# Optimization experiments

Hardware: AMD Instinct MI355X
Metric: run time of the kernel (lower is better)

## Reference

```python
import jax, jax.numpy as jnp
import numpy as np

EMBED_DIM = 512
NUM_HEADS = 8
B, L_Q, L_K = 2, 2048, 2048


def setup_inputs() -> dict:
    key = jax.random.key(0)
    ks = jax.random.split(key, 8)
    s = 0.02  # weight init scale
    return {
        "query": jax.random.normal(ks[0], (B, L_Q, EMBED_DIM), jnp.float32),
        "key":   jax.random.normal(ks[1], (B, L_K, EMBED_DIM), jnp.float32),
        "value": jax.random.normal(ks[2], (B, L_K, EMBED_DIM), jnp.float32),
        "wq": jax.random.normal(ks[3], (EMBED_DIM, EMBED_DIM), jnp.float32) * s,
        "wk": jax.random.normal(ks[4], (EMBED_DIM, EMBED_DIM), jnp.float32) * s,
        "wv": jax.random.normal(ks[5], (EMBED_DIM, EMBED_DIM), jnp.float32) * s,
        "bq": jnp.zeros((EMBED_DIM,), jnp.float32),
        "bk": jnp.zeros((EMBED_DIM,), jnp.float32),
        "bv": jnp.zeros((EMBED_DIM,), jnp.float32),
        "wo": jax.random.normal(ks[6], (EMBED_DIM, EMBED_DIM), jnp.float32) * s,
        "bo": jnp.zeros((EMBED_DIM,), jnp.float32),
    }


def _prob_sparse_mask(query, key, num_heads):
    # Faithful to _prob_QK: max-mean sparsity score, top-k query selection,
    # gather of reduced queries, reduced QK matmul (vectorized, no python loops).
    Bq, Lq, D = query.shape
    Lk = key.shape[1]
    dh = D // num_heads
    n_top = int(np.log(Lk))  # int(np.ceil/np.log) as in source forward: int(np.log(L_K))
    Q = query.reshape(Bq, Lq, num_heads, dh)
    K = key.reshape(Bq, Lk, num_heads, dh)
    Qh = jnp.transpose(Q, (0, 2, 1, 3))                      # [B,H,Lq,dh]
    # NOTE: source does K.transpose(1,2).reshape(B,H,D,L_K) -- a reshape, not a
    # transpose of the last two dims. We replicate that exactly.
    Kr = jnp.transpose(K, (0, 2, 1, 3)).reshape(Bq, num_heads, dh, Lk)  # [B,H,dh,Lk]
    QK = jnp.einsum('bhqd,bhdk->bhqk', Qh, Kr)               # [B,H,Lq,Lk]
    M = QK.max(-1) - QK.sum(-1) / Lk                         # max-mean score [B,H,Lq]
    _, M_top = jax.lax.top_k(M, n_top)                       # [B,H,n_top]
    Q_red = jnp.take_along_axis(Qh, M_top[..., None], axis=2)  # [B,H,n_top,dh]
    QK_red = jnp.einsum('bhtd,bhdk->bhtk', Q_red, Kr)        # [B,H,n_top,Lk]
    # Scatter reduced rows back into a full additive attn mask (zeros elsewhere).
    mask = jnp.zeros((Bq, num_heads, Lq, Lk), QK.dtype)
    bi = jnp.arange(Bq)[:, None, None]
    hi = jnp.arange(num_heads)[None, :, None]
    return mask.at[bi, hi, M_top].set(QK_red)


def reference(query, key, value, wq, wk, wv, bq, bk, bv, wo, bo):
    Bq, Lq, D = query.shape
    Lk = key.shape[1]
    H = NUM_HEADS
    dh = D // H
    mask = _prob_sparse_mask(query, key, H)                  # [B,H,Lq,Lk]
    q = (query @ wq.T + bq).reshape(Bq, Lq, H, dh).transpose(0, 2, 1, 3)
    k = (key @ wk.T + bk).reshape(Bq, Lk, H, dh).transpose(0, 2, 1, 3)
    v = (value @ wv.T + bv).reshape(Bq, Lk, H, dh).transpose(0, 2, 1, 3)
    scores = jnp.einsum('bhqd,bhkd->bhqk', q, k) * (dh ** -0.5) + mask
    attn = jax.nn.softmax(scores, axis=-1)                   # dropout inactive (eval)
    out = jnp.einsum('bhqk,bhkd->bhqd', attn, v)
    out = out.transpose(0, 2, 1, 3).reshape(Bq, Lq, D)
    return out @ wo.T + bo
```

## Files before the change

kernel.cpp:

```cpp
#include <hip/hip_runtime.h>
#include <type_traits>

#define DEV static __device__ __forceinline__

typedef short s16;
typedef __attribute__((ext_vector_type(8))) short short8;
typedef __attribute__((ext_vector_type(4))) float f32x4;
typedef __attribute__((ext_vector_type(16))) float f32x16;

#define NB 2
#define NH 8
#define SL 2048
#define DM 512
#define DH 64
#define NTOP 7
#define NCAND 16
#define LOG2E 1.4426950408889634f
#define NROWS (NB*NH*SL)
#define FSPLIT 4
#define SSPLIT 4

DEV short f2bf(float x){
  union { float f; unsigned u; } v; v.f = x;
  unsigned r = v.u + 0x7fffu + ((v.u >> 16) & 1u);
  return (short)(r >> 16);
}
DEV f32x4 mfma16(short8 a, short8 b, f32x4 c){
  return __builtin_amdgcn_mfma_f32_16x16x32_bf16(a, b, c, 0, 0, 0);
}
DEV f32x16 mfma32(short8 a, short8 b, f32x16 c){
  return __builtin_amdgcn_mfma_f32_32x32x16_bf16(a, b, c, 0, 0, 0);
}
DEV unsigned cvtpk(float lo, float hi){
  unsigned r;
  asm("v_cvt_pk_bf16_f32 %0, %1, %2" : "=v"(r) : "v"(lo), "v"(hi));
  return r;
}
DEV void gl2lds16(const s16* g, s16* l){
  __builtin_amdgcn_global_load_lds(
      (const __attribute__((address_space(1))) unsigned*)g,
      (__attribute__((address_space(3))) unsigned*)l, 16, 0, 0);
}

__global__ void prep_kernel(const float* __restrict__ query, const float* __restrict__ key,
    const float* __restrict__ value,
    const float* __restrict__ wq, const float* __restrict__ wk,
    const float* __restrict__ wv, const float* __restrict__ wo,
    s16* __restrict__ xq, s16* __restrict__ xk, s16* __restrict__ xv,
    s16* __restrict__ khat,
    s16* __restrict__ wqb, s16* __restrict__ wkb, s16* __restrict__ wvb, s16* __restrict__ wob){
  const int nbb = (NB*SL*DM)/256;
  const int wbb = (DM*DM)/256;
  __shared__ s16 thi[64][66];
  int bid = blockIdx.x;
  int t = threadIdx.x;
  if (bid < nbb){ int i = bid*256 + t; xq[i] = f2bf(query[i]); return; }
  bid -= nbb;
  if (bid < nbb){ int i = bid*256 + t; xk[i] = f2bf(key[i]); return; }
  bid -= nbb;
  if (bid < nbb){ int i = bid*256 + t; xv[i] = f2bf(value[i]); return; }
  bid -= nbb;
  if (bid < 512){
    int k6 = bid & 31, h = (bid >> 5) & 7, b = bid >> 8;
    int kl = t & 63, dq = t >> 6;
    #pragma unroll
    for (int dd = 0; dd < 16; ++dd){
      int d = dd*4 + dq;
      thi[d][kl] = f2bf(key[((size_t)b*SL + d*32 + k6)*DM + h*DH + kl]);
    }
    __syncthreads();
    int d2 = t & 63, kq = t >> 6;
    size_t obase = (((size_t)(b*NH + h))*SL + (size_t)k6*64)*DH;
    #pragma unroll
    for (int kk = 0; kk < 16; ++kk){
      int kl2 = kk*4 + kq;
      khat[obase + (size_t)kl2*DH + d2] = thi[d2][kl2];
    }
    return;
  }
  bid -= 512;
  if (bid < wbb){ int i = bid*256 + t; wqb[i] = f2bf(wq[i]); return; }
  bid -= wbb;
  if (bid < wbb){ int i = bid*256 + t; wkb[i] = f2bf(wk[i]); return; }
  bid -= wbb;
  if (bid < wbb){ int i = bid*256 + t; wvb[i] = f2bf(wv[i]); return; }
  bid -= wbb;
  if (bid < wbb){ int i = bid*256 + t; wob[i] = f2bf(wo[i]); return; }
}

__global__ __launch_bounds__(256) void vpt_kernel(const s16* __restrict__ Vp, s16* __restrict__ VpT){
  __shared__ s16 tl[64][66];
  int bid = blockIdx.x;
  int k6 = bid & 31, h = (bid >> 5) & 7, b = bid >> 8;
  int t = threadIdx.x;
  int d = t & 63, kq = t >> 6;
  #pragma unroll
  for (int kk = 0; kk < 16; ++kk){
    int kl = kk*4 + kq;
    tl[kl][d] = Vp[((size_t)b*SL + k6*64 + kl)*DM + h*DH + d];
  }
  __syncthreads();
  int kl2 = t & 63, dq = t >> 6;
  size_t obase = ((size_t)(b*NH + h))*DH*SL + (size_t)k6*64;
  #pragma unroll
  for (int dd = 0; dd < 16; ++dd){
    int d2 = dd*4 + dq;
    VpT[obase + (size_t)d2*SL + kl2] = tl[kl2][d2];
  }
}

template<int OUTF32>
DEV void gemm_body(const s16* __restrict__ A, const s16* __restrict__ Bw,
        const float* __restrict__ bias, void* __restrict__ Cout, int bid, int tid, float scale){
  __shared__ __align__(16) s16 Abuf[2][128*64];
  __shared__ __align__(16) s16 Bbuf[2][64*64];
  int nt = bid >> 3, ot = bid & 7;
  int w = tid >> 6, l = tid & 63;
  int lr = l & 15, lg = l >> 4;
  int n0 = nt*128, o0 = ot*64;
  auto stage = [&](int cur, int kg){
    #pragma unroll
    for (int i = 0; i < 4; ++i){
      int r = w*32 + i*8 + (l>>3);
      int cs = (l&7) ^ (r&7);
      gl2lds16(A + (size_t)(n0 + r)*DM + kg + cs*8, &Abuf[cur][(w*32 + i*8)*64]);
    }
    #pragma unroll
    for (int i = 0; i < 2; ++i){
      int r = w*16 + i*8 + (l>>3);
      int cs = (l&7) ^ (r&7);
      gl2lds16(Bw + (size_t)(o0 + r)*DM + kg + cs*8, &Bbuf[cur][(w*16 + i*8)*64]);
    }
  };
  f32x4 acc[2][4] = {};
  stage(0, 0);
  __syncthreads();
  const int NIT = DM/64;
  for (int it = 0; it < NIT; ++it){
    int cur = it & 1;
    if (it + 1 < NIT) stage(cur^1, (it+1)*64);
    #pragma unroll
    for (int kc = 0; kc < 2; ++kc){
      short8 a0 = *(const short8*)&Abuf[cur][(w*32 +      lr)*64 + ((kc*4+lg) ^ (lr&7))*8];
      short8 a1 = *(const short8*)&Abuf[cur][(w*32 + 16 + lr)*64 + ((kc*4+lg) ^ (lr&7))*8];
      #pragma unroll
      for (int c = 0; c < 4; ++c){
        short8 bf = *(const short8*)&Bbuf[cur][(c*16 + lr)*64 + ((kc*4+lg) ^ (lr&7))*8];
        acc[0][c] = mfma16(a0, bf, acc[0][c]);
        acc[1][c] = mfma16(a1, bf, acc[1][c]);
      }
    }
    __syncthreads();
  }
  #pragma unroll
  for (int sub = 0; sub < 2; ++sub)
    #pragma unroll
    for (int c = 0; c < 4; ++c){
      int col = o0 + c*16 + lr;
      float bb = bias[col];
      #pragma unroll
      for (int j = 0; j < 4; ++j){
        int row = n0 + w*32 + sub*16 + lg*4 + j;
        float v = (acc[sub][c][j] + bb)*scale;
        if (OUTF32) ((float*)Cout)[(size_t)row*DM + col] = v;
        else        ((s16*) Cout)[(size_t)row*DM + col] = f2bf(v);
      }
    }
}

__global__ __launch_bounds__(256) void gemm_proj(const s16* __restrict__ Aq, const s16* __restrict__ Ak,
        const s16* __restrict__ Av, const s16* __restrict__ Wq, const s16* __restrict__ Wk,
        const s16* __restrict__ Wv, const float* __restrict__ bq, const float* __restrict__ bk,
        const float* __restrict__ bv, s16* __restrict__ Oq, s16* __restrict__ Ok, s16* __restrict__ Ov){
  int which = blockIdx.x >> 8;
  const s16* A  = which == 0 ? Aq : which == 1 ? Ak : Av;
  const s16* Bw = which == 0 ? Wq : which == 1 ? Wk : Wv;
  const float* bias = which == 0 ? bq : which == 1 ? bk : bv;
  s16* C = which == 0 ? Oq : which == 1 ? Ok : Ov;
  float scale = which == 0 ? 0.125f*LOG2E : 1.0f;
  gemm_body<0>(A, Bw, bias, C, blockIdx.x & 255, threadIdx.x, scale);
}

__global__ __launch_bounds__(256) void gemm_out(const s16* __restrict__ A, const s16* __restrict__ Bw,
        const float* __restrict__ bias, float* __restrict__ Cout){
  gemm_body<1>(A, Bw, bias, Cout, blockIdx.x, threadIdx.x, 1.0f);
}

__global__ __launch_bounds__(512) void stats_kernel(const s16* __restrict__ xq,
        const s16* __restrict__ khat, float* __restrict__ Mmx, float* __restrict__ Msm){
  __shared__ __align__(16) s16 Hbuf[2][64*64];
  int bid = blockIdx.x;
  int s = bid & 3, qt = (bid >> 2) & 15, h = (bid >> 6) & 7, b = bid >> 9;
  int tid = threadIdx.x;
  int w = tid >> 6, l = tid & 63;
  int lr = l & 15, lg = l >> 4;
  int dx = lr & 7;
  int q0 = qt*128 + w*16;
  const s16* qp = xq + ((size_t)b*SL + q0 + lr)*DM + h*DH + lg*8;
  short8 qh0 = *(const short8*)qp;
  short8 qh1 = *(const short8*)(qp + 32);
  const s16* kb = khat + ((size_t)b*NH + h)*SL*DH;
  const s16* hR0 = &Hbuf[0][lr*64 + ((lg      ^ dx)*8)];
  const s16* hR1 = &Hbuf[0][lr*64 + (((4+lg) ^ dx)*8)];
  int rS = tid >> 3;
  int slot = tid & 7;
  int cs = slot ^ (rS & 7);
  int kbeg = s*(SL/SSPLIT);
  const int NT = (SL/SSPLIT)/64;
  f32x4 hreg;
  auto loadr = [&](int t){
    hreg = *(const f32x4*)(kb + (size_t)(kbeg + t*64 + rS)*DH + cs*8);
  };
  auto writer = [&](int buf){
    *(f32x4*)&Hbuf[buf][rS*64 + slot*8] = hreg;
  };
  float mx = -1e30f, sm = 0.f;
  auto body = [&](auto CURC){
    constexpr int CUR = decltype(CURC)::value;
    #pragma unroll
    for (int t = 0; t < 4; ++t){
      short8 kh0 = *(const short8*)(hR0 + CUR*4096 + t*1024);
      short8 kh1 = *(const short8*)(hR1 + CUR*4096 + t*1024);
      f32x4 sacc = {};
      sacc = mfma16(kh0, qh0, sacc);
      sacc = mfma16(kh1, qh1, sacc);
      #pragma unroll
      for (int j = 0; j < 4; ++j){ mx = fmaxf(mx, sacc[j]); sm += sacc[j]; }
    }
  };
  loadr(0);
  writer(0);
  loadr(1);
  __syncthreads();
  auto step = [&](auto TC){
    constexpr int T = decltype(TC)::value;
    if constexpr (T + 1 < NT) writer((T+1)&1);
    if constexpr (T + 2 < NT) loadr(T+2);
    body(std::integral_constant<int, T&1>{});
    __syncthreads();
  };
  step(std::integral_constant<int,0>{}); step(std::integral_constant<int,1>{});
  step(std::integral_constant<int,2>{}); step(std::integral_constant<int,3>{});
  step(std::integral_constant<int,4>{}); step(std::integral_constant<int,5>{});
  step(std::integral_constant<int,6>{}); step(std::integral_constant<int,7>{});
  mx = fmaxf(mx, __shfl_xor(mx, 16));
  mx = fmaxf(mx, __shfl_xor(mx, 32));
  sm += __shfl_xor(sm, 16);
  sm += __shfl_xor(sm, 32);
  if (lg == 0){
    size_t row = ((size_t)b*NH + h)*SL + q0 + lr;
    Mmx[(size_t)s*NROWS + row] = mx;
    Msm[(size_t)s*NROWS + row] = sm;
  }
}

__global__ __launch_bounds__(256) void topk_kernel(const float* __restrict__ Mmx,
        const float* __restrict__ Msm, int* __restrict__ candidx, int* __restrict__ rowsel){
  int bh = blockIdx.x;
  int t = threadIdx.x;
  int w = t >> 6, l = t & 63;
  __shared__ float smv[SL];
  __shared__ float rv[4];
  __shared__ int   ri[4];
  size_t base = (size_t)bh*SL;
  for (int i = t; i < SL; i += 256){
    float mx = Mmx[base + i];
    float sm = Msm[base + i];
    #pragma unroll
    for (int s = 1; s < SSPLIT; ++s){
      mx = fmaxf(mx, Mmx[(size_t)s*NROWS + base + i]);
      sm += Msm[(size_t)s*NROWS + base + i];
    }
    smv[i] = mx - sm*(1.0f/SL);
    rowsel[base + i] = -1;
  }
  __syncthreads();
  for (int tt = 0; tt < NCAND; ++tt){
    float bvv = -1e38f; int bi = SL;
    for (int i = t; i < SL; i += 256){
      float v = smv[i];
      if (v > bvv){ bvv = v; bi = i; }
    }
    #pragma unroll
    for (int off = 32; off >= 1; off >>= 1){
      float ov = __shfl_xor(bvv, off);
      int oi = __shfl_xor(bi, off);
      if (ov > bvv || (ov == bvv && oi < bi)){ bvv = ov; bi = oi; }
    }
    if (l == 0){ rv[w] = bvv; ri[w] = bi; }
    __syncthreads();
    if (t == 0){
      float bv2 = rv[0]; int bi2 = ri[0];
      #pragma unroll
      for (int ww = 1; ww < 4; ++ww)
        if (rv[ww] > bv2 || (rv[ww] == bv2 && ri[ww] < bi2)){ bv2 = rv[ww]; bi2 = ri[ww]; }
      candidx[bh*NCAND + tt] = bi2;
      smv[bi2] = -1e38f;
    }
    __syncthreads();
  }
}

__global__ __launch_bounds__(256) void cand_kernel(const float* __restrict__ query,
        const float* __restrict__ key, const int* __restrict__ candidx,
        float* __restrict__ candrows, float* __restrict__ cmx, float* __restrict__ csm){
  __shared__ float tile[64][65];
  __shared__ float qs[NCAND][64];
  int bid = blockIdx.x;
  int k6 = bid & 31, h = (bid >> 5) & 7, b = bid >> 8;
  int bh = b*NH + h;
  int t = threadIdx.x;
  int kl = t & 63, w = t >> 6;
  for (int i = t; i < NCAND*64; i += 256){
    int tt = i >> 6, d = i & 63;
    qs[tt][d] = query[((size_t)b*SL + candidx[bh*NCAND + tt])*DM + h*DH + d];
  }
  #pragma unroll
  for (int dd = 0; dd < 16; ++dd){
    int d = dd*4 + w;
    tile[d][kl] = key[((size_t)b*SL + d*32 + k6)*DM + h*DH + kl];
  }
  __syncthreads();
  for (int tt = w; tt < NCAND; tt += 4){
    float acc = 0.f;
    #pragma unroll
    for (int d = 0; d < 64; ++d)
      acc = fmaf(qs[tt][d], tile[d][kl], acc);
    candrows[((size_t)bh*NCAND + tt)*SL + k6*64 + kl] = acc*LOG2E;
    float mx = acc, sm = acc;
    #pragma unroll
    for (int off = 1; off < 64; off <<= 1){
      mx = fmaxf(mx, __shfl_xor(mx, off));
      sm += __shfl_xor(sm, off);
    }
    if (kl == 0){
      cmx[((size_t)bh*NCAND + tt)*32 + k6] = mx;
      csm[((size_t)bh*NCAND + tt)*32 + k6] = sm;
    }
  }
}

__global__ __launch_bounds__(64) void topsel_kernel(const float* __restrict__ cmx,
        const float* __restrict__ csm, const int* __restrict__ candidx, int* __restrict__ rowsel){
  int bh = blockIdx.x;
  int l = threadIdx.x;
  __shared__ float Mex[NCAND];
  if (l < NCAND){
    float mx = -1e38f, sm = 0.f;
    #pragma unroll 4
    for (int p = 0; p < 32; ++p){
      mx = fmaxf(mx, cmx[((size_t)bh*NCAND + l)*32 + p]);
      sm += csm[((size_t)bh*NCAND + l)*32 + p];
    }
    Mex[l] = mx - sm*(1.0f/SL);
  }
  __syncthreads();
  if (l == 0){
    unsigned used = 0;
    for (int tt = 0; tt < NTOP; ++tt){
      float bv = -1e38f; int bslot = 0; int brow = 1 << 30;
      for (int c = 0; c < NCAND; ++c){
        if (used & (1u << c)) continue;
        int row = candidx[bh*NCAND + c];
        float v = Mex[c];
        if (v > bv || (v == bv && row < brow)){ bv = v; bslot = c; brow = row; }
      }
      used |= 1u << bslot;
      rowsel[(size_t)bh*SL + brow] = bslot;
    }
  }
}

__global__ __launch_bounds__(256, 3) void flash_kernel(const s16* __restrict__ Qp,
        const s16* __restrict__ Kp, const s16* __restrict__ VpT,
        const float* __restrict__ candrows, const int* __restrict__ rowsel,
        float* __restrict__ Opart, float* __restrict__ lpart){
  __shared__ __align__(16) s16 SB[4*64*64];
  int bid = blockIdx.x;
  int s = bid & 3, qt = (bid >> 2) & 15, h = (bid >> 6) & 7, b = bid >> 9;
  int tid = threadIdx.x;
  int w = tid >> 6, l = tid & 63;
  int ln = l & 31, lh = l >> 5;
  int q0 = qt*128 + w*32;
  int bh = b*NH + h;
  const s16* qp = Qp + ((size_t)b*SL + q0 + ln)*DM + h*DH + lh*8;
  short8 bq[4];
  #pragma unroll
  for (int kc = 0; kc < 4; ++kc) bq[kc] = *(const short8*)(qp + kc*16);
  int sel = rowsel[(size_t)bh*SL + q0 + ln];
  const float* mrow = candrows + ((size_t)bh*NCAND + (sel >= 0 ? sel : 0))*SL;
  const s16* kpb = Kp + (size_t)b*SL*DM + h*DH;
  const s16* vtb = VpT + (size_t)bh*DH*SL;
  const s16* kR[2][4];
  #pragma unroll
  for (int g = 0; g < 2; ++g)
    #pragma unroll
    for (int kc = 0; kc < 4; ++kc)
      kR[g][kc] = &SB[(g*32 + ln)*64 + ((((kc*2 + lh) ^ (ln & 7) ^ ((ln >> 3) & 3))*8))];
  int r8 = l >> 3;
  int slot = l & 7;
  int cs = slot ^ r8 ^ w;
  int kbeg = s*(SL/FSPLIT);
  const int NT = (SL/FSPLIT)/64;
  f32x4 kreg[2], vreg[2];
  auto loadr = [&](int t){
    int kg = kbeg + t*64;
    #pragma unroll
    for (int c = 0; c < 2; ++c){
      int r = c*32 + w*8 + r8;
      kreg[c] = *(const f32x4*)(kpb + (size_t)(kg + r)*DM + cs*8);
      vreg[c] = *(const f32x4*)(vtb + (size_t)r*SL + kg + cs*8);
    }
  };
  auto writer = [&](int buf){
    #pragma unroll
    for (int c = 0; c < 2; ++c){
      int r = c*32 + w*8 + r8;
      *(f32x4*)&SB[(size_t)buf*4096 + r*64 + slot*8] = kreg[c];
      *(f32x4*)&SB[8192 + (size_t)buf*4096 + r*64 + slot*8] = vreg[c];
    }
  };
  short8 ones;
  #pragma unroll
  for (int i = 0; i < 8; ++i) ones[i] = (short)0x3F80;
  f32x16 accO[2] = {};
  f32x16 accL = {};
  auto body = [&](auto CURC, int k0){
    constexpr int CB = decltype(CURC)::value * 8192;
    f32x16 S[2] = {};
    __builtin_amdgcn_s_setprio(1);
    #pragma unroll
    for (int g = 0; g < 2; ++g)
      #pragma unroll
      for (int kc = 0; kc < 4; ++kc){
        short8 kf = *(const short8*)((const char*)kR[g][kc] + CB);
        S[g] = mfma32(kf, bq[kc], S[g]);
      }
    __builtin_amdgcn_s_setprio(0);
    if (sel >= 0){
      #pragma unroll
      for (int g = 0; g < 2; ++g)
        #pragma unroll
        for (int rq = 0; rq < 4; ++rq)
          #pragma unroll
          for (int j = 0; j < 4; ++j)
            S[g][rq*4 + j] += mrow[k0 + g*32 + rq*8 + lh*4 + j];
    }
    #pragma unroll
    for (int g = 0; g < 2; ++g)
      #pragma unroll
      for (int e = 0; e < 16; ++e)
        S[g][e] = exp2f(S[g][e]);
    unsigned W[2][8];
    #pragma unroll
    for (int g = 0; g < 2; ++g)
      #pragma unroll
      for (int t = 0; t < 8; ++t)
        W[g][t] = cvtpk(S[g][2*t], S[g][2*t+1]);
    short8 pf[4];
    #pragma unroll
    for (int kc = 0; kc < 4; ++kc){
      int g = kc >> 1, j = kc & 1;
      unsigned a0 = W[g][4*j + 0], a1 = W[g][4*j + 2];
      asm("v_permlane32_swap_b32 %0, %1" : "+v"(a0), "+v"(a1));
      unsigned b0 = W[g][4*j + 1], b1 = W[g][4*j + 3];
      asm("v_permlane32_swap_b32 %0, %1" : "+v"(b0), "+v"(b1));
      union { unsigned u[4]; short8 s8; } uu;
      uu.u[0] = a0; uu.u[1] = b0; uu.u[2] = a1; uu.u[3] = b1;
      pf[kc] = uu.s8;
    }
    __builtin_amdgcn_s_setprio(1);
    #pragma unroll
    for (int kc = 0; kc < 4; ++kc)
      accL = mfma32(ones, pf[kc], accL);
    #pragma unroll
    for (int dg = 0; dg < 2; ++dg)
      #pragma unroll
      for (int kc = 0; kc < 4; ++kc){
        short8 vf = *(const short8*)((const char*)kR[dg][kc] + CB + 16384);
        accO[dg] = mfma32(vf, pf[kc], accO[dg]);
      }
    __builtin_amdgcn_s_setprio(0);
  };
  loadr(0);
  writer(0);
  loadr(1);
  __syncthreads();
  auto step = [&](auto TC){
    constexpr int T = decltype(TC)::value;
    if constexpr (T + 1 < NT) writer((T+1)&1);
    if constexpr (T + 2 < NT) loadr(T+2);
    body(std::integral_constant<int, T&1>{}, kbeg + T*64);
    __syncthreads();
  };
  step(std::integral_constant<int,0>{}); step(std::integral_constant<int,1>{});
  step(std::integral_constant<int,2>{}); step(std::integral_constant<int,3>{});
  step(std::integral_constant<int,4>{}); step(std::integral_constant<int,5>{});
  step(std::integral_constant<int,6>{}); step(std::integral_constant<int,7>{});
  size_t row = (size_t)bh*SL + q0 + ln;
  float* Op = Opart + ((size_t)s*NROWS + row)*DH;
  #pragma unroll
  for (int dg = 0; dg < 2; ++dg)
    #pragma unroll
    for (int rq = 0; rq < 4; ++rq){
      f32x4 v = { accO[dg][rq*4+0], accO[dg][rq*4+1], accO[dg][rq*4+2], accO[dg][rq*4+3] };
      *(f32x4*)(Op + dg*32 + rq*8 + lh*4) = v;
    }
  if (lh == 0)
    lpart[(size_t)s*NROWS + row] = accL[0];
}

__global__ __launch_bounds__(256) void flash_combine(const float* __restrict__ Opart,
        const float* __restrict__ lpart, s16* __restrict__ outh){
  int row = blockIdx.x*4 + (threadIdx.x >> 6);
  int d = threadIdx.x & 63;
  float L = 0.f, o = 0.f;
  #pragma unroll
  for (int s = 0; s < FSPLIT; ++s){
    L += lpart[(size_t)s*NROWS + row];
    o += Opart[((size_t)s*NROWS + row)*DH + d];
  }
  o /= L;
  int b = row >> 14, h = (row >> 11) & 7, q = row & (SL - 1);
  outh[((size_t)b*SL + q)*DM + h*DH + d] = f2bf(o);
}

extern "C" void kernel_launch(void* const* d_in, const int* in_sizes, int n_in,
                              void* d_out, int out_size, void* d_ws, size_t ws_size,
                              hipStream_t stream){
  (void)in_sizes; (void)n_in; (void)out_size;
  const float* query = (const float*)d_in[0];
  const float* key   = (const float*)d_in[1];
  const float* value = (const float*)d_in[2];
  const float* wq    = (const float*)d_in[3];
  const float* wk    = (const float*)d_in[4];
  const float* wv    = (const float*)d_in[5];
  const float* bq    = (const float*)d_in[6];
  const float* bk    = (const float*)d_in[7];
  const float* bv    = (const float*)d_in[8];
  const float* wo    = (const float*)d_in[9];
  const float* bo    = (const float*)d_in[10];

  const size_t NE = (size_t)NB*SL*DM;
  const size_t WE = (size_t)DM*DM;

  char* p = (char*)d_ws;
  size_t off = 0;
  auto alloc = [&](size_t n)->char*{ char* r = p + off; off += (n + 255) & ~(size_t)255; return r; };
  s16* wob = (s16*)alloc(WE*2);
  s16* Qp  = (s16*)alloc(NE*2);
  s16* Kp  = (s16*)alloc(NE*2);
  s16* VpT = (s16*)alloc(NE*2);
  float* candrows = (float*)alloc((size_t)NB*NH*NCAND*SL*4);
  int* candidx  = (int*)alloc((size_t)NB*NH*NCAND*4);
  float* cmx    = (float*)alloc((size_t)NB*NH*NCAND*32*4);
  float* csm    = (float*)alloc((size_t)NB*NH*NCAND*32*4);
  int* rowsel   = (int*)alloc((size_t)NROWS*4);
  float* Mmx    = (float*)alloc((size_t)SSPLIT*NROWS*4);
  float* Msm    = (float*)alloc((size_t)SSPLIT*NROWS*4);
  float* lpart  = (float*)alloc((size_t)FSPLIT*NROWS*4);
  float* Opart  = (float*)alloc((size_t)FSPLIT*NROWS*DH*4);
  s16* outh = (s16*)alloc(NE*2);
  s16* xq   = (s16*)alloc(NE*2);
  s16* xk   = (s16*)alloc(NE*2);
  s16* xv   = (s16*)alloc(NE*2);
  s16* khat = (s16*)alloc(NE*2);
  s16* wqb = (s16*)alloc(WE*2);
  s16* wkb = (s16*)alloc(WE*2);
  s16* wvb = (s16*)alloc(WE*2);
  s16* Vp  = (s16*)alloc(NE*2);
  if (off > ws_size) return;

  const int nbb = (int)(NE/256);
  const int wbb = (int)(WE/256);
  prep_kernel<<<3*nbb + 512 + 4*wbb, 256, 0, stream>>>(query, key, value, wq, wk, wv, wo,
      xq, xk, xv, khat, wqb, wkb, wvb, wob);

  gemm_proj<<<3*256, 256, 0, stream>>>(xq, xk, xv, wqb, wkb, wvb, bq, bk, bv, Qp, Kp, Vp);
  vpt_kernel<<<512, 256, 0, stream>>>(Vp, VpT);

  stats_kernel<<<NB*NH*(SL/128)*SSPLIT, 512, 0, stream>>>(xq, khat, Mmx, Msm);
  topk_kernel<<<NB*NH, 256, 0, stream>>>(Mmx, Msm, candidx, rowsel);
  cand_kernel<<<512, 256, 0, stream>>>(query, key, candidx, candrows, cmx, csm);
  topsel_kernel<<<NB*NH, 64, 0, stream>>>(cmx, csm, candidx, rowsel);

  flash_kernel<<<NB*NH*(SL/128)*FSPLIT, 256, 0, stream>>>(Qp, Kp, VpT, candrows, rowsel,
      Opart, lpart);
  flash_combine<<<NROWS/4, 256, 0, stream>>>(Opart, lpart, outh);
  gemm_out<<<256, 256, 0, stream>>>(outh, wob, bo, (float*)d_out);
}
```

Baseline: 149.2 us.

## Halve flash key split, register-resident top-k, rolled pipeline loop

Reduces the flash attention key split from 4 to 2 partitions, so there are half as many blocks, each processing twice as many key tiles. This halves the Opart/lpart traffic the combine kernel must read, at the cost of fewer blocks to fill the GPU. The main loop becomes a rolled two-stage double-buffered loop instead of a fully unrolled sequence. The top-k kernel keeps scores in registers and rescans only the winning thread's values each round instead of rescanning shared memory, and workspace buffers are reordered.

```diff
diff --git a/kernel.cpp b/kernel.cpp
--- a/kernel.cpp
+++ b/kernel.cpp
@@ -17,7 +17,7 @@
 #define NCAND 16
 #define LOG2E 1.4426950408889634f
 #define NROWS (NB*NH*SL)
-#define FSPLIT 4
+#define FSPLIT 2
 #define SSPLIT 4
 
 DEV short f2bf(float x){
@@ -259,11 +259,14 @@
   int bh = blockIdx.x;
   int t = threadIdx.x;
   int w = t >> 6, l = t & 63;
-  __shared__ float smv[SL];
-  __shared__ float rv[4];
-  __shared__ int   ri[4];
+  __shared__ float bval[4];
+  __shared__ int   bidx[4];
+  __shared__ int   gsel;
   size_t base = (size_t)bh*SL;
-  for (int i = t; i < SL; i += 256){
+  float v[8];
+  #pragma unroll
+  for (int j = 0; j < 8; ++j){
+    int i = j*256 + t;
     float mx = Mmx[base + i];
     float sm = Msm[base + i];
     #pragma unroll
@@ -271,33 +274,40 @@
       mx = fmaxf(mx, Mmx[(size_t)s*NROWS + base + i]);
       sm += Msm[(size_t)s*NROWS + base + i];
     }
-    smv[i] = mx - sm*(1.0f/SL);
+    v[j] = mx - sm*(1.0f/SL);
     rowsel[base + i] = -1;
   }
-  __syncthreads();
+  float lv = -1e38f; int li = SL;
+  #pragma unroll
+  for (int j = 0; j < 8; ++j)
+    if (v[j] > lv){ lv = v[j]; li = j*256 + t; }
   for (int tt = 0; tt < NCAND; ++tt){
-    float bvv = -1e38f; int bi = SL;
-    for (int i = t; i < SL; i += 256){
-      float v = smv[i];
-      if (v > bvv){ bvv = v; bi = i; }
-    }
+    float cv = lv; int ci = li;
     #pragma unroll
     for (int off = 32; off >= 1; off >>= 1){
-      float ov = __shfl_xor(bvv, off);
-      int oi = __shfl_xor(bi, off);
-      if (ov > bvv || (ov == bvv && oi < bi)){ bvv = ov; bi = oi; }
-    }
-    if (l == 0){ rv[w] = bvv; ri[w] = bi; }
+      float ov = __shfl_xor(cv, off);
+      int oi = __shfl_xor(ci, off);
+      if (ov > cv || (ov == cv && oi < ci)){ cv = ov; ci = oi; }
+    }
+    if (l == 0){ bval[w] = cv; bidx[w] = ci; }
     __syncthreads();
     if (t == 0){
-      float bv2 = rv[0]; int bi2 = ri[0];
+      float bv2 = bval[0]; int bi2 = bidx[0];
       #pragma unroll
       for (int ww = 1; ww < 4; ++ww)
-        if (rv[ww] > bv2 || (rv[ww] == bv2 && ri[ww] < bi2)){ bv2 = rv[ww]; bi2 = ri[ww]; }
+        if (bval[ww] > bv2 || (bval[ww] == bv2 && bidx[ww] < bi2)){ bv2 = bval[ww]; bi2 = bidx[ww]; }
       candidx[bh*NCAND + tt] = bi2;
-      smv[bi2] = -1e38f;
+      gsel = bi2;
     }
     __syncthreads();
+    int win = gsel;
+    if ((win & 255) == t){
+      v[win >> 8] = -1e38f;
+      lv = -1e38f; li = SL;
+      #pragma unroll
+      for (int j = 0; j < 8; ++j)
+        if (v[j] > lv){ lv = v[j]; li = j*256 + t; }
+    }
   }
 }
 
@@ -377,7 +387,7 @@
         float* __restrict__ Opart, float* __restrict__ lpart){
   __shared__ __align__(16) s16 SB[4*64*64];
   int bid = blockIdx.x;
-  int s = bid & 3, qt = (bid >> 2) & 15, h = (bid >> 6) & 7, b = bid >> 9;
+  int s = bid & 1, qt = (bid >> 1) & 15, h = (bid >> 5) & 7, b = bid >> 8;
   int tid = threadIdx.x;
   int w = tid >> 6, l = tid & 63;
   int ln = l & 31, lh = l >> 5;
@@ -401,7 +411,6 @@
   int slot = l & 7;
   int cs = slot ^ r8 ^ w;
   int kbeg = s*(SL/FSPLIT);
-  const int NT = (SL/FSPLIT)/64;
   f32x4 kreg[2], vreg[2];
   auto loadr = [&](int t){
     int kg = kbeg + t*64;
@@ -486,17 +495,18 @@
   writer(0);
   loadr(1);
   __syncthreads();
-  auto step = [&](auto TC){
-    constexpr int T = decltype(TC)::value;
-    if constexpr (T + 1 < NT) writer((T+1)&1);
-    if constexpr (T + 2 < NT) loadr(T+2);
-    body(std::integral_constant<int, T&1>{}, kbeg + T*64);
+  const int NT = (SL/FSPLIT)/64;
+  #pragma unroll 1
+  for (int i2 = 0; i2 < NT/2; ++i2){
+    writer(1);
+    if (2*i2 + 2 < NT) loadr(2*i2 + 2);
+    body(std::integral_constant<int,0>{}, kbeg + (2*i2)*64);
     __syncthreads();
-  };
-  step(std::integral_constant<int,0>{}); step(std::integral_constant<int,1>{});
-  step(std::integral_constant<int,2>{}); step(std::integral_constant<int,3>{});
-  step(std::integral_constant<int,4>{}); step(std::integral_constant<int,5>{});
-  step(std::integral_constant<int,6>{}); step(std::integral_constant<int,7>{});
+    if (2*i2 + 2 < NT) writer(0);
+    if (2*i2 + 3 < NT) loadr(2*i2 + 3);
+    body(std::integral_constant<int,1>{}, kbeg + (2*i2+1)*64);
+    __syncthreads();
+  }
   size_t row = (size_t)bh*SL + q0 + ln;
   float* Op = Opart + ((size_t)s*NROWS + row)*DH;
   #pragma unroll
@@ -547,10 +557,19 @@
   char* p = (char*)d_ws;
   size_t off = 0;
   auto alloc = [&](size_t n)->char*{ char* r = p + off; off += (n + 255) & ~(size_t)255; return r; };
-  s16* wob = (s16*)alloc(WE*2);
   s16* Qp  = (s16*)alloc(NE*2);
   s16* Kp  = (s16*)alloc(NE*2);
+  s16* Vp  = (s16*)alloc(NE*2);
   s16* VpT = (s16*)alloc(NE*2);
+  s16* khat = (s16*)alloc(NE*2);
+  s16* outh = (s16*)alloc(NE*2);
+  s16* xq   = (s16*)alloc(NE*2);
+  s16* xk   = (s16*)alloc(NE*2);
+  s16* xv   = (s16*)alloc(NE*2);
+  s16* wqb = (s16*)alloc(WE*2);
+  s16* wkb = (s16*)alloc(WE*2);
+  s16* wvb = (s16*)alloc(WE*2);
+  s16* wob = (s16*)alloc(WE*2);
   float* candrows = (float*)alloc((size_t)NB*NH*NCAND*SL*4);
   int* candidx  = (int*)alloc((size_t)NB*NH*NCAND*4);
   float* cmx    = (float*)alloc((size_t)NB*NH*NCAND*32*4);
@@ -560,15 +579,6 @@
   float* Msm    = (float*)alloc((size_t)SSPLIT*NROWS*4);
   float* lpart  = (float*)alloc((size_t)FSPLIT*NROWS*4);
   float* Opart  = (float*)alloc((size_t)FSPLIT*NROWS*DH*4);
-  s16* outh = (s16*)alloc(NE*2);
-  s16* xq   = (s16*)alloc(NE*2);
-  s16* xk   = (s16*)alloc(NE*2);
-  s16* xv   = (s16*)alloc(NE*2);
-  s16* khat = (s16*)alloc(NE*2);
-  s16* wqb = (s16*)alloc(WE*2);
-  s16* wkb = (s16*)alloc(WE*2);
-  s16* wvb = (s16*)alloc(WE*2);
-  s16* Vp  = (s16*)alloc(NE*2);
   if (off > ws_size) return;
 
   const int nbb = (int)(NE/256);
```

After: 145.9 us. 1.02x faster.
